# Kernel optimization log

Measured on AMD Instinct MI355X. Metric: run time of the kernel, lower is better.

## Reference

```python
import jax, jax.numpy as jnp
import numpy as np

N = 100000   # nodes
E = 1600000  # edges (avg degree 16)
F = 128      # in_feats == h_feats
G = 64       # graphs in batch
EPS = 1e-5   # GraphNorm eps


def setup_inputs() -> dict:
    key = jax.random.key(0)
    ks = jax.random.split(key, 9)
    inputs = jax.random.normal(ks[0], (N, F), dtype=jnp.float32)
    edge_index = jax.random.randint(ks[1], (2, E), 0, N, dtype=jnp.int32)
    batch = jnp.sort(jax.random.randint(ks[2], (N,), 0, G, dtype=jnp.int32))
    edge_weight = jax.random.uniform(ks[3], (E,), dtype=jnp.float32)
    scale = 1.0 / np.sqrt(F)
    W = jax.random.normal(ks[4], (F, F), dtype=jnp.float32) * scale
    b = jax.random.normal(ks[5], (F,), dtype=jnp.float32) * scale
    gn_weight = jnp.ones((F,), dtype=jnp.float32)
    gn_bias = jnp.zeros((F,), dtype=jnp.float32)
    gn_mean_scale = jnp.ones((F,), dtype=jnp.float32)
    return {"inputs": inputs, "edge_index": edge_index, "batch": batch,
            "edge_weight": edge_weight, "W": W, "b": b,
            "gn_weight": gn_weight, "gn_bias": gn_bias,
            "gn_mean_scale": gn_mean_scale}


def _gcn_block(inputs, edge_index, batch, edge_weight, W, b,
               gn_weight, gn_bias, gn_mean_scale):
    # --- GCNConv (PyG defaults: add self-loops, symmetric norm) ---
    src, dst = edge_index[0], edge_index[1]
    loop = jnp.arange(N, dtype=src.dtype)
    src_f = jnp.concatenate([src, loop])
    dst_f = jnp.concatenate([dst, loop])
    ew_f = jnp.concatenate([edge_weight, jnp.ones((N,), edge_weight.dtype)])
    deg = jax.ops.segment_sum(ew_f, dst_f, num_segments=N)
    dis = jnp.where(deg > 0, jax.lax.rsqrt(jnp.maximum(deg, 1e-30)), 0.0)
    norm = dis[src_f] * ew_f * dis[dst_f]                    # [E+N]
    xw = inputs @ W                                          # [N, F]
    msgs = norm[:, None] * xw[src_f]                         # [E+N, F]
    h = jax.ops.segment_sum(msgs, dst_f, num_segments=N) + b # [N, F]

    # --- GraphNorm (per-graph mean/std with learnable mean_scale) ---
    cnt = jnp.maximum(jax.ops.segment_sum(jnp.ones((N,), h.dtype), batch,
                                          num_segments=G), 1.0)  # [G]
    mean = jax.ops.segment_sum(h, batch, num_segments=G) / cnt[:, None]
    out = h - mean[batch] * gn_mean_scale
    var = jax.ops.segment_sum(out * out, batch, num_segments=G) / cnt[:, None]
    std = jnp.sqrt(var + EPS)
    h = gn_weight * out / std[batch] + gn_bias

    # --- ReLU, then global max pool over each graph ---
    h_emb = jax.nn.relu(h)
    flat = jax.ops.segment_max(h_emb, batch, num_segments=G)  # [G, F]
    return h_emb, flat


def reference(inputs, edge_index, batch, edge_weight, W, b,
              gn_weight, gn_bias, gn_mean_scale):
    h_emb, flat = _gcn_block(inputs, edge_index, batch, edge_weight, W, b,
                             gn_weight, gn_bias, gn_mean_scale)
    return (h_emb, flat, edge_index, edge_weight, batch)
```

## Files before the change

kernel.cpp:

```cpp
#include <hip/hip_runtime.h>

#define NN 100000
#define NE 1600000
#define FF 128
#define NG 64
#define GN_EPS 1e-5f
#define SLOT 64

typedef unsigned int uint;
typedef unsigned long long ull;
typedef unsigned short ushort;
typedef __attribute__((ext_vector_type(8))) short short8;
typedef __attribute__((ext_vector_type(4))) float f32x4;

__device__ __forceinline__ float bflo(uint u) { return __uint_as_float(u << 16); }
__device__ __forceinline__ float bfhi(uint u) { return __uint_as_float(u & 0xffff0000u); }
__device__ __forceinline__ uint f2bf1(float a) {
    uint ua = __float_as_uint(a);
    return (ua + 0x7fffu + ((ua >> 16) & 1u)) >> 16;
}
__device__ __forceinline__ uint f2bf_pack(float a, float b) {
    return f2bf1(a) | (f2bf1(b) << 16);
}

__global__ void k_init(ull* pk, float* sum1, float* sum2, int* flat_i) {
    int i = blockIdx.x * blockDim.x + threadIdx.x;
    if (i < NN) pk[i] = 0ULL;
    if (i < NG * FF) { sum1[i] = 0.f; sum2[i] = 0.f; flat_i[i] = 0; }
}

__global__ void k_deg(const int* __restrict__ ei, const float* __restrict__ ew,
                      ull* __restrict__ pk, uint* __restrict__ eslot) {
    int e = blockIdx.x * blockDim.x + threadIdx.x;
    if (e < NE) {
        int s = ei[e];
        int d = ei[NE + e];
        float w = ew[e];
        ull fx = (ull)(w * 4294967296.0f);
        ull old = atomicAdd(&pk[d], (1ULL << 48) | fx);
        int r = (int)(old >> 48);
        uint entry = ((uint)s << 15) | (uint)__float2int_rn(w * 32767.0f);
        if (r < SLOT)
            __builtin_nontemporal_store(entry, &eslot[(size_t)d * SLOT + r]);
    }
}

__global__ void k_dis(const ull* __restrict__ pk, float* __restrict__ dis,
                      int* __restrict__ indeg, const int* __restrict__ batch,
                      int* __restrict__ gstart) {
    int i = blockIdx.x * blockDim.x + threadIdx.x;
    if (i >= NN) return;
    ull p = pk[i];
    float deg = 1.0f + (float)((double)(p & 0xFFFFFFFFFFFFULL) * (1.0 / 4294967296.0));
    dis[i] = rsqrtf(deg);
    int c = (int)(p >> 48);
    indeg[i] = c < SLOT ? c : SLOT;
    int b = batch[i];
    int prev = (i == 0) ? -1 : batch[i - 1];
    for (int g = prev + 1; g <= b; g++) gstart[g] = i;
    if (i == NN - 1) { for (int g = b + 1; g <= NG; g++) gstart[g] = NN; }
}

__global__ void k_wcvt(const float* __restrict__ W, uint4* __restrict__ wb) {
    int t = blockIdx.x * blockDim.x + threadIdx.x;
    if (t >= 2048) return;
    int tile = t >> 6, l = t & 63;
    int nt = tile >> 2, kt = tile & 3;
    int j = nt * 16 + (l & 15);
    int kb = kt * 32 + (l >> 4) * 8;
    uint u[4];
    #pragma unroll
    for (int p = 0; p < 4; p++) {
        float e0 = W[(size_t)(kb + 2 * p + 0) * FF + j];
        float e1 = W[(size_t)(kb + 2 * p + 1) * FF + j];
        u[p] = f2bf_pack(e0, e1);
    }
    wb[t] = make_uint4(u[0], u[1], u[2], u[3]);
}

__global__ __launch_bounds__(256) void k_gemm(const float* __restrict__ A,
                                              const uint4* __restrict__ wb,
                                              const float* __restrict__ dis,
                                              uint* __restrict__ xwh) {
    __shared__ uint4 wlds[2048];
    int t = threadIdx.x;
    for (int i = t; i < 2048; i += 256) wlds[i] = wb[i];
    __syncthreads();

    int wave = t >> 6, lane = t & 63;
    int kg = lane >> 4;
    int row = blockIdx.x * 64 + wave * 16 + (lane & 15);
    int rowc = row < NN ? row : NN - 1;

    const float4* A4 = (const float4*)A;
    short8 afrag[4];
    #pragma unroll
    for (int kt = 0; kt < 4; kt++) {
        float4 pq0 = A4[(size_t)rowc * 32 + kt * 8 + kg * 2 + 0];
        float4 pq1 = A4[(size_t)rowc * 32 + kt * 8 + kg * 2 + 1];
        uint u0 = f2bf_pack(pq0.x, pq0.y);
        uint u1 = f2bf_pack(pq0.z, pq0.w);
        uint u2 = f2bf_pack(pq1.x, pq1.y);
        uint u3 = f2bf_pack(pq1.z, pq1.w);
        short8 f;
        f[0] = (short)(u0 & 0xffff); f[1] = (short)(u0 >> 16);
        f[2] = (short)(u1 & 0xffff); f[3] = (short)(u1 >> 16);
        f[4] = (short)(u2 & 0xffff); f[5] = (short)(u2 >> 16);
        f[6] = (short)(u3 & 0xffff); f[7] = (short)(u3 >> 16);
        afrag[kt] = f;
    }

    f32x4 acc[8];
    #pragma unroll
    for (int nt = 0; nt < 8; nt++) acc[nt] = (f32x4){0.f, 0.f, 0.f, 0.f};

    #pragma unroll
    for (int nt = 0; nt < 8; nt++) {
        #pragma unroll
        for (int kt = 0; kt < 4; kt++) {
            short8 bfrag = *(const short8*)&wlds[(nt * 4 + kt) * 64 + lane];
            acc[nt] = __builtin_amdgcn_mfma_f32_16x16x32_bf16(afrag[kt], bfrag, acc[nt], 0, 0, 0);
        }
    }

    float dv[4];
    #pragma unroll
    for (int r = 0; r < 4; r++) {
        int rout = blockIdx.x * 64 + wave * 16 + kg * 4 + r;
        dv[r] = (rout < NN) ? dis[rout] : 0.f;
    }
    ushort* xs = (ushort*)xwh;
    int col0 = lane & 15;
    #pragma unroll
    for (int nt = 0; nt < 8; nt++) {
        #pragma unroll
        for (int r = 0; r < 4; r++) {
            int rout = blockIdx.x * 64 + wave * 16 + kg * 4 + r;
            if (rout < NN)
                xs[(size_t)rout * FF + nt * 16 + col0] = (ushort)f2bf1(acc[nt][r] * dv[r]);
        }
    }
}

__global__ __launch_bounds__(256) void k_agg(const int* __restrict__ indeg,
                                             const uint* __restrict__ eslot,
                                             const uint* __restrict__ xwh,
                                             const float* __restrict__ dis,
                                             const float* __restrict__ bias,
                                             uint* __restrict__ h32) {
    int wid = (blockIdx.x * blockDim.x + threadIdx.x) >> 6;
    int lane = threadIdx.x & 63;
    if (wid >= NN) return;
    int cnt = indeg[wid];
    float dd = dis[wid];
    uint us = xwh[(size_t)wid * 64 + lane];
    float px = bflo(us), py = bfhi(us);
    const uint* base = eslot + (size_t)wid * SLOT;
    const float qs = 1.0f / 32767.0f;
    int i = 0;
    for (; i + 3 < cnt; i += 4) {
        uint4 pp = *(const uint4*)&base[i];
        uint u0 = xwh[(size_t)(pp.x >> 15) * 64 + lane];
        uint u1 = xwh[(size_t)(pp.y >> 15) * 64 + lane];
        uint u2 = xwh[(size_t)(pp.z >> 15) * 64 + lane];
        uint u3 = xwh[(size_t)(pp.w >> 15) * 64 + lane];
        float w0 = (float)(pp.x & 0x7fff) * qs;
        float w1 = (float)(pp.y & 0x7fff) * qs;
        float w2 = (float)(pp.z & 0x7fff) * qs;
        float w3 = (float)(pp.w & 0x7fff) * qs;
        px += w0 * bflo(u0); py += w0 * bfhi(u0);
        px += w1 * bflo(u1); py += w1 * bfhi(u1);
        px += w2 * bflo(u2); py += w2 * bfhi(u2);
        px += w3 * bflo(u3); py += w3 * bfhi(u3);
    }
    for (; i < cnt; i++) {
        uint p0 = base[i];
        uint u0 = xwh[(size_t)(p0 >> 15) * 64 + lane];
        float w0 = (float)(p0 & 0x7fff) * qs;
        px += w0 * bflo(u0); py += w0 * bfhi(u0);
    }
    float2 bb = ((const float2*)bias)[lane];
    h32[(size_t)wid * 64 + lane] = f2bf_pack(bb.x + dd * px, bb.y + dd * py);
}

__global__ __launch_bounds__(256) void k_gsums(const uint* __restrict__ h32,
                                               const int* __restrict__ gstart,
                                               float* __restrict__ sum1,
                                               float* __restrict__ sum2) {
    __shared__ float s1a[256], s1b[256], s2a[256], s2b[256];
    int g = blockIdx.x >> 3;
    int s = blockIdx.x & 7;
    int t = threadIdx.x;
    int f2 = t & 63;
    int half = t >> 6;
    int a = gstart[g], b = gstart[g + 1];
    float x0 = 0.f, x1 = 0.f, y0 = 0.f, y1 = 0.f;
    for (int n = a + s * 4 + half; n < b; n += 32) {
        uint u = h32[(size_t)n * 64 + f2];
        float v0 = bflo(u), v1 = bfhi(u);
        x0 += v0; x1 += v1; y0 += v0 * v0; y1 += v1 * v1;
    }
    s1a[t] = x0; s1b[t] = x1; s2a[t] = y0; s2b[t] = y1;
    __syncthreads();
    if (half == 0) {
        for (int j = 1; j < 4; j++) {
            x0 += s1a[t + j * 64]; x1 += s1b[t + j * 64];
            y0 += s2a[t + j * 64]; y1 += s2b[t + j * 64];
        }
        atomicAdd(&sum1[g * FF + f2 * 2 + 0], x0);
        atomicAdd(&sum1[g * FF + f2 * 2 + 1], x1);
        atomicAdd(&sum2[g * FF + f2 * 2 + 0], y0);
        atomicAdd(&sum2[g * FF + f2 * 2 + 1], y1);
    }
}

__global__ void k_gstats(const float* sum1, const float* sum2, const int* gstart,
                         const float* ms, float* cfac, float* istd) {
    int i = blockIdx.x * blockDim.x + threadIdx.x;
    if (i >= NG * FF) return;
    int g = i >> 7, f = i & 127;
    float cnt = (float)max(gstart[g + 1] - gstart[g], 1);
    float mean = sum1[i] / cnt;
    float c = mean * ms[f];
    float var = sum2[i] / cnt - 2.f * c * mean + c * c;
    var = fmaxf(var, 0.f);
    cfac[i] = c;
    istd[i] = rsqrtf(var + GN_EPS);
}

__global__ __launch_bounds__(256) void k_final(const uint* __restrict__ h32,
                                               const int* __restrict__ batch,
                                               const float* __restrict__ cfac,
                                               const float* __restrict__ istd,
                                               const float* __restrict__ gw,
                                               const float* __restrict__ gb,
                                               float* __restrict__ out,
                                               int* __restrict__ flat_i) {
    __shared__ float sm[8][FF];
    __shared__ int gg[8];
    int t = threadIdx.x;
    int n0 = blockIdx.x * 8;
    int rq = t >> 5;
    int q = t & 31;
    int n = n0 + rq;
    if (t < 8) gg[t] = batch[n0 + t];
    int g = batch[n];
    int fq = q * 4;
    uint2 hu = *(const uint2*)&h32[(size_t)n * 64 + q * 2];
    float4 h4 = { bflo(hu.x), bfhi(hu.x), bflo(hu.y), bfhi(hu.y) };
    float4 c4 = *(const float4*)&cfac[g * FF + fq];
    float4 s4 = *(const float4*)&istd[g * FF + fq];
    float4 w4 = *(const float4*)&gw[fq];
    float4 b4 = *(const float4*)&gb[fq];
    float4 y;
    y.x = fmaxf(w4.x * (h4.x - c4.x) * s4.x + b4.x, 0.f);
    y.y = fmaxf(w4.y * (h4.y - c4.y) * s4.y + b4.y, 0.f);
    y.z = fmaxf(w4.z * (h4.z - c4.z) * s4.z + b4.z, 0.f);
    y.w = fmaxf(w4.w * (h4.w - c4.w) * s4.w + b4.w, 0.f);
    *(float4*)&out[(size_t)n * FF + fq] = y;
    *(float4*)&sm[rq][fq] = y;
    __syncthreads();
    if (t < FF) {
        int f = t;
        int gprev = gg[0];
        float m = 0.f;
        for (int r = 0; r < 8; r++) {
            int gr = gg[r];
            if (gr != gprev) {
                atomicMax(&flat_i[gprev * FF + f], __float_as_int(m));
                m = 0.f; gprev = gr;
            }
            m = fmaxf(m, sm[r][f]);
        }
        atomicMax(&flat_i[gprev * FF + f], __float_as_int(m));
    }
}

__global__ void k_copy(const int4* __restrict__ ei4, const float4* __restrict__ ew4,
                       const int4* __restrict__ b4, float* __restrict__ out_tail) {
    int i = blockIdx.x * blockDim.x + threadIdx.x;
    if (i < 2 * NE / 4) {
        int4 v = ei4[i];
        float4 o = { (float)v.x, (float)v.y, (float)v.z, (float)v.w };
        *(float4*)&out_tail[(size_t)i * 4] = o;
    } else if (i < 2 * NE / 4 + NE / 4) {
        int j = i - 2 * NE / 4;
        *(float4*)&out_tail[2 * NE + (size_t)j * 4] = ew4[j];
    } else if (i < 2 * NE / 4 + NE / 4 + NN / 4) {
        int j = i - (2 * NE / 4 + NE / 4);
        int4 v = b4[j];
        float4 o = { (float)v.x, (float)v.y, (float)v.z, (float)v.w };
        *(float4*)&out_tail[3 * NE + (size_t)j * 4] = o;
    }
}

extern "C" void kernel_launch(void* const* d_in, const int* in_sizes, int n_in,
                              void* d_out, int out_size, void* d_ws, size_t ws_size,
                              hipStream_t stream) {
    const float* inputs = (const float*)d_in[0];
    const int*   ei     = (const int*)d_in[1];
    const int*   batch  = (const int*)d_in[2];
    const float* ew     = (const float*)d_in[3];
    const float* W      = (const float*)d_in[4];
    const float* bias   = (const float*)d_in[5];
    const float* gnw    = (const float*)d_in[6];
    const float* gnb    = (const float*)d_in[7];
    const float* ms     = (const float*)d_in[8];
    float* out = (float*)d_out;

    char* p = (char*)d_ws;
    uint* xwh    = (uint*)p;  p += (size_t)NN * 64 * 4;
    uint* h32    = (uint*)p;  p += (size_t)NN * 64 * 4;
    uint* eslot  = (uint*)p;  p += (size_t)NN * SLOT * 4;
    ull* pk      = (ull*)p;   p += (size_t)NN * 8;
    float* dis   = (float*)p; p += (size_t)NN * 4;
    float* sum1  = (float*)p; p += (size_t)NG * FF * 4;
    float* sum2  = (float*)p; p += (size_t)NG * FF * 4;
    float* cfac  = (float*)p; p += (size_t)NG * FF * 4;
    float* istd  = (float*)p; p += (size_t)NG * FF * 4;
    int* indeg   = (int*)p;   p += (size_t)NN * 4;
    int* gstart  = (int*)p;   p += (size_t)(NG + 1) * 4;
    uint4* wb    = (uint4*)p; p += 2048 * 16;

    const int TB = 256;
    int nblkN  = (NN + TB - 1) / TB;
    int nblkE  = (NE + TB - 1) / TB;

    float* out_hemb = out;
    float* out_flat = out + (size_t)NN * FF;
    float* out_tail = out_flat + (size_t)NG * FF;
    int*   flat_i   = (int*)out_flat;

    k_init<<<nblkN, TB, 0, stream>>>(pk, sum1, sum2, flat_i);
    k_deg<<<nblkE, TB, 0, stream>>>(ei, ew, pk, eslot);
    k_dis<<<nblkN, TB, 0, stream>>>(pk, dis, indeg, batch, gstart);
    k_wcvt<<<8, 256, 0, stream>>>(W, wb);
    k_gemm<<<(NN + 63) / 64, 256, 0, stream>>>(inputs, wb, dis, xwh);
    k_agg<<<NN / 4, 256, 0, stream>>>(indeg, eslot, xwh, dis, bias, h32);
    k_gsums<<<NG * 8, 256, 0, stream>>>(h32, gstart, sum1, sum2);
    k_gstats<<<(NG * FF + TB - 1) / TB, TB, 0, stream>>>(sum1, sum2, gstart, ms, cfac, istd);
    k_final<<<NN / 8, 256, 0, stream>>>(h32, batch, cfac, istd, gnw, gnb, out_hemb, flat_i);
    k_copy<<<(2 * NE / 4 + NE / 4 + NN / 4 + TB - 1) / TB, TB, 0, stream>>>(
        (const int4*)ei, (const float4*)ew, (const int4*)batch, out_tail);
}
```

Baseline: 391.7 us.

## Replace global atomics with partial buffers and 32-bit degree counters

Degree accumulation now uses a 32-bit counter atomic, and the degree is recomputed from the quantized weights stored in the edge slots instead of a packed 64-bit fixed-point atomic. Per-graph sums are written to per-block partial buffers and reduced in the stats kernel, replacing float atomics. The fused max-pool in the final kernel is split into a separate two-stage reduction that rereads the output embedding. This removes atomics but adds two launches, a full extra read of the 51MB output, and slightly different degree precision, since the quantized weights drop edges beyond SLOT.

```diff
diff --git a/kernel.cpp b/kernel.cpp
--- a/kernel.cpp
+++ b/kernel.cpp
@@ -23,38 +23,38 @@
     return f2bf1(a) | (f2bf1(b) << 16);
 }
 
-__global__ void k_init(ull* pk, float* sum1, float* sum2, int* flat_i) {
-    int i = blockIdx.x * blockDim.x + threadIdx.x;
-    if (i < NN) pk[i] = 0ULL;
-    if (i < NG * FF) { sum1[i] = 0.f; sum2[i] = 0.f; flat_i[i] = 0; }
+__global__ void k_init(uint* cnt) {
+    int i = blockIdx.x * blockDim.x + threadIdx.x;
+    if (i < NN) cnt[i] = 0u;
 }
 
 __global__ void k_deg(const int* __restrict__ ei, const float* __restrict__ ew,
-                      ull* __restrict__ pk, uint* __restrict__ eslot) {
+                      uint* __restrict__ cnt, uint* __restrict__ eslot) {
     int e = blockIdx.x * blockDim.x + threadIdx.x;
     if (e < NE) {
         int s = ei[e];
         int d = ei[NE + e];
         float w = ew[e];
-        ull fx = (ull)(w * 4294967296.0f);
-        ull old = atomicAdd(&pk[d], (1ULL << 48) | fx);
-        int r = (int)(old >> 48);
+        uint r = atomicAdd(&cnt[d], 1u);
         uint entry = ((uint)s << 15) | (uint)__float2int_rn(w * 32767.0f);
         if (r < SLOT)
             __builtin_nontemporal_store(entry, &eslot[(size_t)d * SLOT + r]);
     }
 }
 
-__global__ void k_dis(const ull* __restrict__ pk, float* __restrict__ dis,
-                      int* __restrict__ indeg, const int* __restrict__ batch,
-                      int* __restrict__ gstart) {
+__global__ void k_dis(const uint* __restrict__ cnt, const uint* __restrict__ eslot,
+                      float* __restrict__ dis, int* __restrict__ indeg,
+                      const int* __restrict__ batch, int* __restrict__ gstart) {
     int i = blockIdx.x * blockDim.x + threadIdx.x;
     if (i >= NN) return;
-    ull p = pk[i];
-    float deg = 1.0f + (float)((double)(p & 0xFFFFFFFFFFFFULL) * (1.0 / 4294967296.0));
-    dis[i] = rsqrtf(deg);
-    int c = (int)(p >> 48);
-    indeg[i] = c < SLOT ? c : SLOT;
+    uint c0 = cnt[i];
+    int c = c0 < SLOT ? (int)c0 : SLOT;
+    indeg[i] = c;
+    const uint* base = eslot + (size_t)i * SLOT;
+    float s = 0.f;
+    const float qs = 1.0f / 32767.0f;
+    for (int j = 0; j < c; j++) s += (float)(base[j] & 0x7fff);
+    dis[i] = rsqrtf(1.0f + s * qs);
     int b = batch[i];
     int prev = (i == 0) ? -1 : batch[i - 1];
     for (int g = prev + 1; g <= b; g++) gstart[g] = i;
@@ -185,8 +185,8 @@
 
 __global__ __launch_bounds__(256) void k_gsums(const uint* __restrict__ h32,
                                                const int* __restrict__ gstart,
-                                               float* __restrict__ sum1,
-                                               float* __restrict__ sum2) {
+                                               float* __restrict__ psum1,
+                                               float* __restrict__ psum2) {
     __shared__ float s1a[256], s1b[256], s2a[256], s2b[256];
     int g = blockIdx.x >> 3;
     int s = blockIdx.x & 7;
@@ -207,22 +207,28 @@
             x0 += s1a[t + j * 64]; x1 += s1b[t + j * 64];
             y0 += s2a[t + j * 64]; y1 += s2b[t + j * 64];
         }
-        atomicAdd(&sum1[g * FF + f2 * 2 + 0], x0);
-        atomicAdd(&sum1[g * FF + f2 * 2 + 1], x1);
-        atomicAdd(&sum2[g * FF + f2 * 2 + 0], y0);
-        atomicAdd(&sum2[g * FF + f2 * 2 + 1], y1);
-    }
-}
-
-__global__ void k_gstats(const float* sum1, const float* sum2, const int* gstart,
-                         const float* ms, float* cfac, float* istd) {
+        int bse = blockIdx.x * FF + f2 * 2;
+        psum1[bse + 0] = x0; psum1[bse + 1] = x1;
+        psum2[bse + 0] = y0; psum2[bse + 1] = y1;
+    }
+}
+
+__global__ void k_gstats(const float* __restrict__ psum1, const float* __restrict__ psum2,
+                         const int* gstart, const float* ms,
+                         float* cfac, float* istd) {
     int i = blockIdx.x * blockDim.x + threadIdx.x;
     if (i >= NG * FF) return;
     int g = i >> 7, f = i & 127;
-    float cnt = (float)max(gstart[g + 1] - gstart[g], 1);
-    float mean = sum1[i] / cnt;
+    float s1 = 0.f, s2 = 0.f;
+    #pragma unroll
+    for (int s = 0; s < 8; s++) {
+        s1 += psum1[(g * 8 + s) * FF + f];
+        s2 += psum2[(g * 8 + s) * FF + f];
+    }
+    float cntf = (float)max(gstart[g + 1] - gstart[g], 1);
+    float mean = s1 / cntf;
     float c = mean * ms[f];
-    float var = sum2[i] / cnt - 2.f * c * mean + c * c;
+    float var = s2 / cntf - 2.f * c * mean + c * c;
     var = fmaxf(var, 0.f);
     cfac[i] = c;
     istd[i] = rsqrtf(var + GN_EPS);
@@ -234,18 +240,13 @@
                                                const float* __restrict__ istd,
                                                const float* __restrict__ gw,
                                                const float* __restrict__ gb,
-                                               float* __restrict__ out,
-                                               int* __restrict__ flat_i) {
-    __shared__ float sm[8][FF];
-    __shared__ int gg[8];
-    int t = threadIdx.x;
-    int n0 = blockIdx.x * 8;
-    int rq = t >> 5;
-    int q = t & 31;
-    int n = n0 + rq;
-    if (t < 8) gg[t] = batch[n0 + t];
+                                               float* __restrict__ out) {
+    int i = blockIdx.x * blockDim.x + threadIdx.x;
+    if (i >= NN * 32) return;
+    int n = i >> 5;
+    int q = i & 31;
+    int fq = q * 4;
     int g = batch[n];
-    int fq = q * 4;
     uint2 hu = *(const uint2*)&h32[(size_t)n * 64 + q * 2];
     float4 h4 = { bflo(hu.x), bfhi(hu.x), bflo(hu.y), bfhi(hu.y) };
     float4 c4 = *(const float4*)&cfac[g * FF + fq];
@@ -258,22 +259,35 @@
     y.z = fmaxf(w4.z * (h4.z - c4.z) * s4.z + b4.z, 0.f);
     y.w = fmaxf(w4.w * (h4.w - c4.w) * s4.w + b4.w, 0.f);
     *(float4*)&out[(size_t)n * FF + fq] = y;
-    *(float4*)&sm[rq][fq] = y;
+}
+
+__global__ __launch_bounds__(256) void k_gmax(const float* __restrict__ hemb,
+                                              const int* __restrict__ gstart,
+                                              float* __restrict__ pmax) {
+    __shared__ float sm[256];
+    int g = blockIdx.x >> 3;
+    int s = blockIdx.x & 7;
+    int t = threadIdx.x;
+    int f = t & 127, rr = t >> 7;
+    int a = gstart[g], b = gstart[g + 1];
+    float m = 0.f;
+    for (int n = a + s * 2 + rr; n < b; n += 16)
+        m = fmaxf(m, hemb[(size_t)n * FF + f]);
+    sm[t] = m;
     __syncthreads();
-    if (t < FF) {
-        int f = t;
-        int gprev = gg[0];
-        float m = 0.f;
-        for (int r = 0; r < 8; r++) {
-            int gr = gg[r];
-            if (gr != gprev) {
-                atomicMax(&flat_i[gprev * FF + f], __float_as_int(m));
-                m = 0.f; gprev = gr;
-            }
-            m = fmaxf(m, sm[r][f]);
-        }
-        atomicMax(&flat_i[gprev * FF + f], __float_as_int(m));
-    }
+    if (rr == 0)
+        pmax[blockIdx.x * FF + f] = fmaxf(sm[t], sm[t + 128]);
+}
+
+__global__ void k_gmax2(const float* __restrict__ pmax, float* __restrict__ flat) {
+    int i = blockIdx.x * blockDim.x + threadIdx.x;
+    if (i >= NG * FF) return;
+    int g = i >> 7, f = i & 127;
+    float m = 0.f;
+    #pragma unroll
+    for (int s = 0; s < 8; s++)
+        m = fmaxf(m, pmax[(g * 8 + s) * FF + f]);
+    flat[i] = m;
 }
 
 __global__ void k_copy(const int4* __restrict__ ei4, const float4* __restrict__ ew4,
@@ -312,10 +326,11 @@
     uint* xwh    = (uint*)p;  p += (size_t)NN * 64 * 4;
     uint* h32    = (uint*)p;  p += (size_t)NN * 64 * 4;
     uint* eslot  = (uint*)p;  p += (size_t)NN * SLOT * 4;
-    ull* pk      = (ull*)p;   p += (size_t)NN * 8;
+    uint* cnt    = (uint*)p;  p += (size_t)NN * 4;
     float* dis   = (float*)p; p += (size_t)NN * 4;
-    float* sum1  = (float*)p; p += (size_t)NG * FF * 4;
-    float* sum2  = (float*)p; p += (size_t)NG * FF * 4;
+    float* psum1 = (float*)p; p += (size_t)NG * 8 * FF * 4;
+    float* psum2 = (float*)p; p += (size_t)NG * 8 * FF * 4;
+    float* pmax  = (float*)p; p += (size_t)NG * 8 * FF * 4;
     float* cfac  = (float*)p; p += (size_t)NG * FF * 4;
     float* istd  = (float*)p; p += (size_t)NG * FF * 4;
     int* indeg   = (int*)p;   p += (size_t)NN * 4;
@@ -329,17 +344,18 @@
     float* out_hemb = out;
     float* out_flat = out + (size_t)NN * FF;
     float* out_tail = out_flat + (size_t)NG * FF;
-    int*   flat_i   = (int*)out_flat;
-
-    k_init<<<nblkN, TB, 0, stream>>>(pk, sum1, sum2, flat_i);
-    k_deg<<<nblkE, TB, 0, stream>>>(ei, ew, pk, eslot);
-    k_dis<<<nblkN, TB, 0, stream>>>(pk, dis, indeg, batch, gstart);
+
+    k_init<<<nblkN, TB, 0, stream>>>(cnt);
+    k_deg<<<nblkE, TB, 0, stream>>>(ei, ew, cnt, eslot);
+    k_dis<<<nblkN, TB, 0, stream>>>(cnt, eslot, dis, indeg, batch, gstart);
     k_wcvt<<<8, 256, 0, stream>>>(W, wb);
     k_gemm<<<(NN + 63) / 64, 256, 0, stream>>>(inputs, wb, dis, xwh);
     k_agg<<<NN / 4, 256, 0, stream>>>(indeg, eslot, xwh, dis, bias, h32);
-    k_gsums<<<NG * 8, 256, 0, stream>>>(h32, gstart, sum1, sum2);
-    k_gstats<<<(NG * FF + TB - 1) / TB, TB, 0, stream>>>(sum1, sum2, gstart, ms, cfac, istd);
-    k_final<<<NN / 8, 256, 0, stream>>>(h32, batch, cfac, istd, gnw, gnb, out_hemb, flat_i);
+    k_gsums<<<NG * 8, 256, 0, stream>>>(h32, gstart, psum1, psum2);
+    k_gstats<<<(NG * FF + TB - 1) / TB, TB, 0, stream>>>(psum1, psum2, gstart, ms, cfac, istd);
+    k_final<<<(NN * 32 + TB - 1) / TB, TB, 0, stream>>>(h32, batch, cfac, istd, gnw, gnb, out_hemb);
+    k_gmax<<<NG * 8, 256, 0, stream>>>(out_hemb, gstart, pmax);
+    k_gmax2<<<(NG * FF + TB - 1) / TB, TB, 0, stream>>>(pmax, out_flat);
     k_copy<<<(2 * NE / 4 + NE / 4 + NN / 4 + TB - 1) / TB, TB, 0, stream>>>(
         (const int4*)ei, (const float4*)ew, (const int4*)batch, out_tail);
 }
```

Measured after the change: 407.2 us. 4.0% more time.

## Replace global per-node atomics with two-pass bucketed edge partition for CSR build

Applied to the files above, without the earlier changes.

Builds the padded per-destination edge lists in two passes. First, edges are binned by destination block of 128 nodes into a staging buffer using LDS histograms and one global atomic per bucket per block. Then each bucket is scattered locally with LDS atomics. Degree is now recomputed from the quantized slot weights instead of 64-bit fixed-point atomics, and the W conversion is folded into k_dis. GraphNorm sums are written as partials instead of float atomics, which makes them deterministic. The costs are an extra pass over the staging buffer, which aliases h32, and a degree that is wrong if a bucket overflows CAP or a node has more than 64 in-edges.

```diff
diff --git a/kernel.cpp b/kernel.cpp
--- a/kernel.cpp
+++ b/kernel.cpp
@@ -6,9 +6,11 @@
 #define NG 64
 #define GN_EPS 1e-5f
 #define SLOT 64
+#define NB 782
+#define CAP 2560
+#define PBLK 256
 
 typedef unsigned int uint;
-typedef unsigned long long ull;
 typedef unsigned short ushort;
 typedef __attribute__((ext_vector_type(8))) short short8;
 typedef __attribute__((ext_vector_type(4))) float f32x4;
@@ -23,59 +25,95 @@
     return f2bf1(a) | (f2bf1(b) << 16);
 }
 
-__global__ void k_init(ull* pk, float* sum1, float* sum2, int* flat_i) {
-    int i = blockIdx.x * blockDim.x + threadIdx.x;
-    if (i < NN) pk[i] = 0ULL;
-    if (i < NG * FF) { sum1[i] = 0.f; sum2[i] = 0.f; flat_i[i] = 0; }
-}
-
-__global__ void k_deg(const int* __restrict__ ei, const float* __restrict__ ew,
-                      ull* __restrict__ pk, uint* __restrict__ eslot) {
-    int e = blockIdx.x * blockDim.x + threadIdx.x;
-    if (e < NE) {
+__global__ __launch_bounds__(256) void k_part(const int* __restrict__ ei,
+                                              const float* __restrict__ ew,
+                                              uint* __restrict__ gfill,
+                                              uint2* __restrict__ ebuf) {
+    __shared__ uint hist[1024], base[1024];
+    int tid = threadIdx.x;
+    int e0 = blockIdx.x * (NE / PBLK);
+    int e1 = e0 + (NE / PBLK);
+    for (int c = tid; c < 1024; c += 256) hist[c] = 0;
+    __syncthreads();
+    for (int e = e0 + tid; e < e1; e += 256) {
+        int d = ei[NE + e];
+        atomicAdd(&hist[d >> 7], 1u);
+    }
+    __syncthreads();
+    for (int c = tid; c < 1024; c += 256) {
+        uint h = hist[c];
+        base[c] = (c < NB && h) ? atomicAdd(&gfill[c * 16], h) : 0u;
+        hist[c] = 0;
+    }
+    __syncthreads();
+    for (int e = e0 + tid; e < e1; e += 256) {
         int s = ei[e];
         int d = ei[NE + e];
         float w = ew[e];
-        ull fx = (ull)(w * 4294967296.0f);
-        ull old = atomicAdd(&pk[d], (1ULL << 48) | fx);
-        int r = (int)(old >> 48);
-        uint entry = ((uint)s << 15) | (uint)__float2int_rn(w * 32767.0f);
+        int b = d >> 7;
+        uint r = atomicAdd(&hist[b], 1u);
+        uint pos = base[b] + r;
+        if (pos < CAP)
+            ebuf[(size_t)b * CAP + pos] =
+                make_uint2((uint)s | ((uint)(d & 127) << 17), __float_as_uint(w));
+    }
+}
+
+__global__ __launch_bounds__(256) void k_build(const uint* __restrict__ gfill,
+                                               const uint2* __restrict__ ebuf,
+                                               uint* __restrict__ eslot,
+                                               uint* __restrict__ cnt) {
+    __shared__ uint lcnt[128];
+    int b = blockIdx.x;
+    int tid = threadIdx.x;
+    if (tid < 128) lcnt[tid] = 0;
+    __syncthreads();
+    uint m = gfill[b * 16]; if (m > CAP) m = CAP;
+    int n0 = b << 7;
+    for (uint i = tid; i < m; i += 256) {
+        uint2 en = ebuf[(size_t)b * CAP + i];
+        uint src = en.x & 0x1FFFFu;
+        uint dlo = (en.x >> 17) & 127u;
+        float w = __uint_as_float(en.y);
+        uint r = atomicAdd(&lcnt[dlo], 1u);
         if (r < SLOT)
-            __builtin_nontemporal_store(entry, &eslot[(size_t)d * SLOT + r]);
-    }
-}
-
-__global__ void k_dis(const ull* __restrict__ pk, float* __restrict__ dis,
-                      int* __restrict__ indeg, const int* __restrict__ batch,
-                      int* __restrict__ gstart) {
+            eslot[(size_t)(n0 + dlo) * SLOT + r] =
+                (src << 15) | (uint)__float2int_rn(w * 32767.0f);
+    }
+    __syncthreads();
+    if (tid < 128 && n0 + tid < NN) cnt[n0 + tid] = lcnt[tid];
+}
+
+__global__ void k_dis(const uint* __restrict__ cnt, const uint* __restrict__ eslot,
+                      float* __restrict__ dis, const int* __restrict__ batch,
+                      int* __restrict__ gstart, const float* __restrict__ W,
+                      uint4* __restrict__ wb) {
     int i = blockIdx.x * blockDim.x + threadIdx.x;
+    if (i < 2048) {
+        int tile = i >> 6, l = i & 63;
+        int nt = tile >> 2, kt = tile & 3;
+        int j = nt * 16 + (l & 15);
+        int kb = kt * 32 + (l >> 4) * 8;
+        uint u[4];
+        #pragma unroll
+        for (int p = 0; p < 4; p++) {
+            float e0 = W[(size_t)(kb + 2 * p + 0) * FF + j];
+            float e1 = W[(size_t)(kb + 2 * p + 1) * FF + j];
+            u[p] = f2bf_pack(e0, e1);
+        }
+        wb[i] = make_uint4(u[0], u[1], u[2], u[3]);
+    }
     if (i >= NN) return;
-    ull p = pk[i];
-    float deg = 1.0f + (float)((double)(p & 0xFFFFFFFFFFFFULL) * (1.0 / 4294967296.0));
-    dis[i] = rsqrtf(deg);
-    int c = (int)(p >> 48);
-    indeg[i] = c < SLOT ? c : SLOT;
+    uint c0 = cnt[i];
+    int c = c0 < SLOT ? (int)c0 : SLOT;
+    const uint* base = eslot + (size_t)i * SLOT;
+    float s = 0.f;
+    for (int j = 0; j < c; j++) s += (float)(base[j] & 0x7fff);
+    dis[i] = rsqrtf(1.0f + s * (1.0f / 32767.0f));
     int b = batch[i];
     int prev = (i == 0) ? -1 : batch[i - 1];
     for (int g = prev + 1; g <= b; g++) gstart[g] = i;
     if (i == NN - 1) { for (int g = b + 1; g <= NG; g++) gstart[g] = NN; }
-}
-
-__global__ void k_wcvt(const float* __restrict__ W, uint4* __restrict__ wb) {
-    int t = blockIdx.x * blockDim.x + threadIdx.x;
-    if (t >= 2048) return;
-    int tile = t >> 6, l = t & 63;
-    int nt = tile >> 2, kt = tile & 3;
-    int j = nt * 16 + (l & 15);
-    int kb = kt * 32 + (l >> 4) * 8;
-    uint u[4];
-    #pragma unroll
-    for (int p = 0; p < 4; p++) {
-        float e0 = W[(size_t)(kb + 2 * p + 0) * FF + j];
-        float e1 = W[(size_t)(kb + 2 * p + 1) * FF + j];
-        u[p] = f2bf_pack(e0, e1);
-    }
-    wb[t] = make_uint4(u[0], u[1], u[2], u[3]);
 }
 
 __global__ __launch_bounds__(256) void k_gemm(const float* __restrict__ A,
@@ -142,7 +180,7 @@
     }
 }
 
-__global__ __launch_bounds__(256) void k_agg(const int* __restrict__ indeg,
+__global__ __launch_bounds__(256) void k_agg(const uint* __restrict__ cnt,
                                              const uint* __restrict__ eslot,
                                              const uint* __restrict__ xwh,
                                              const float* __restrict__ dis,
@@ -151,14 +189,15 @@
     int wid = (blockIdx.x * blockDim.x + threadIdx.x) >> 6;
     int lane = threadIdx.x & 63;
     if (wid >= NN) return;
-    int cnt = indeg[wid];
+    uint c0 = cnt[wid];
+    int c = c0 < SLOT ? (int)c0 : SLOT;
     float dd = dis[wid];
     uint us = xwh[(size_t)wid * 64 + lane];
     float px = bflo(us), py = bfhi(us);
     const uint* base = eslot + (size_t)wid * SLOT;
     const float qs = 1.0f / 32767.0f;
     int i = 0;
-    for (; i + 3 < cnt; i += 4) {
+    for (; i + 3 < c; i += 4) {
         uint4 pp = *(const uint4*)&base[i];
         uint u0 = xwh[(size_t)(pp.x >> 15) * 64 + lane];
         uint u1 = xwh[(size_t)(pp.y >> 15) * 64 + lane];
@@ -173,7 +212,7 @@
         px += w2 * bflo(u2); py += w2 * bfhi(u2);
         px += w3 * bflo(u3); py += w3 * bfhi(u3);
     }
-    for (; i < cnt; i++) {
+    for (; i < c; i++) {
         uint p0 = base[i];
         uint u0 = xwh[(size_t)(p0 >> 15) * 64 + lane];
         float w0 = (float)(p0 & 0x7fff) * qs;
@@ -185,8 +224,8 @@
 
 __global__ __launch_bounds__(256) void k_gsums(const uint* __restrict__ h32,
                                                const int* __restrict__ gstart,
-                                               float* __restrict__ sum1,
-                                               float* __restrict__ sum2) {
+                                               float* __restrict__ psum1,
+                                               float* __restrict__ psum2) {
     __shared__ float s1a[256], s1b[256], s2a[256], s2b[256];
     int g = blockIdx.x >> 3;
     int s = blockIdx.x & 7;
@@ -207,22 +246,28 @@
             x0 += s1a[t + j * 64]; x1 += s1b[t + j * 64];
             y0 += s2a[t + j * 64]; y1 += s2b[t + j * 64];
         }
-        atomicAdd(&sum1[g * FF + f2 * 2 + 0], x0);
-        atomicAdd(&sum1[g * FF + f2 * 2 + 1], x1);
-        atomicAdd(&sum2[g * FF + f2 * 2 + 0], y0);
-        atomicAdd(&sum2[g * FF + f2 * 2 + 1], y1);
-    }
-}
-
-__global__ void k_gstats(const float* sum1, const float* sum2, const int* gstart,
-                         const float* ms, float* cfac, float* istd) {
+        int bse = blockIdx.x * FF + f2 * 2;
+        psum1[bse + 0] = x0; psum1[bse + 1] = x1;
+        psum2[bse + 0] = y0; psum2[bse + 1] = y1;
+    }
+}
+
+__global__ void k_gstats(const float* __restrict__ psum1, const float* __restrict__ psum2,
+                         const int* gstart, const float* ms,
+                         float* cfac, float* istd) {
     int i = blockIdx.x * blockDim.x + threadIdx.x;
     if (i >= NG * FF) return;
     int g = i >> 7, f = i & 127;
-    float cnt = (float)max(gstart[g + 1] - gstart[g], 1);
-    float mean = sum1[i] / cnt;
+    float s1 = 0.f, s2 = 0.f;
+    #pragma unroll
+    for (int s = 0; s < 8; s++) {
+        s1 += psum1[(g * 8 + s) * FF + f];
+        s2 += psum2[(g * 8 + s) * FF + f];
+    }
+    float cntf = (float)max(gstart[g + 1] - gstart[g], 1);
+    float mean = s1 / cntf;
     float c = mean * ms[f];
-    float var = sum2[i] / cnt - 2.f * c * mean + c * c;
+    float var = s2 / cntf - 2.f * c * mean + c * c;
     var = fmaxf(var, 0.f);
     cfac[i] = c;
     istd[i] = rsqrtf(var + GN_EPS);
@@ -310,35 +355,36 @@
 
     char* p = (char*)d_ws;
     uint* xwh    = (uint*)p;  p += (size_t)NN * 64 * 4;
-    uint* h32    = (uint*)p;  p += (size_t)NN * 64 * 4;
+    uint* h32    = (uint*)p;
+    uint2* ebuf  = (uint2*)p; p += (size_t)NN * 64 * 4;
     uint* eslot  = (uint*)p;  p += (size_t)NN * SLOT * 4;
-    ull* pk      = (ull*)p;   p += (size_t)NN * 8;
+    uint* gfill  = (uint*)p;  p += (size_t)1024 * 16 * 4;
+    uint* cnt    = (uint*)p;  p += (size_t)NN * 4;
     float* dis   = (float*)p; p += (size_t)NN * 4;
-    float* sum1  = (float*)p; p += (size_t)NG * FF * 4;
-    float* sum2  = (float*)p; p += (size_t)NG * FF * 4;
+    float* psum1 = (float*)p; p += (size_t)NG * 8 * FF * 4;
+    float* psum2 = (float*)p; p += (size_t)NG * 8 * FF * 4;
     float* cfac  = (float*)p; p += (size_t)NG * FF * 4;
     float* istd  = (float*)p; p += (size_t)NG * FF * 4;
-    int* indeg   = (int*)p;   p += (size_t)NN * 4;
     int* gstart  = (int*)p;   p += (size_t)(NG + 1) * 4;
     uint4* wb    = (uint4*)p; p += 2048 * 16;
 
     const int TB = 256;
-    int nblkN  = (NN + TB - 1) / TB;
-    int nblkE  = (NE + TB - 1) / TB;
+    int nblkN = (NN + TB - 1) / TB;
 
     float* out_hemb = out;
     float* out_flat = out + (size_t)NN * FF;
     float* out_tail = out_flat + (size_t)NG * FF;
     int*   flat_i   = (int*)out_flat;
 
-    k_init<<<nblkN, TB, 0, stream>>>(pk, sum1, sum2, flat_i);
-    k_deg<<<nblkE, TB, 0, stream>>>(ei, ew, pk, eslot);
-    k_dis<<<nblkN, TB, 0, stream>>>(pk, dis, indeg, batch, gstart);
-    k_wcvt<<<8, 256, 0, stream>>>(W, wb);
+    hipMemsetAsync(gfill, 0, 1024 * 16 * 4, stream);
+    hipMemsetAsync(flat_i, 0, NG * FF * 4, stream);
+    k_part<<<PBLK, 256, 0, stream>>>(ei, ew, gfill, ebuf);
+    k_build<<<NB, 256, 0, stream>>>(gfill, ebuf, eslot, cnt);
+    k_dis<<<nblkN, TB, 0, stream>>>(cnt, eslot, dis, batch, gstart, W, wb);
     k_gemm<<<(NN + 63) / 64, 256, 0, stream>>>(inputs, wb, dis, xwh);
-    k_agg<<<NN / 4, 256, 0, stream>>>(indeg, eslot, xwh, dis, bias, h32);
-    k_gsums<<<NG * 8, 256, 0, stream>>>(h32, gstart, sum1, sum2);
-    k_gstats<<<(NG * FF + TB - 1) / TB, TB, 0, stream>>>(sum1, sum2, gstart, ms, cfac, istd);
+    k_agg<<<NN / 4, 256, 0, stream>>>(cnt, eslot, xwh, dis, bias, h32);
+    k_gsums<<<NG * 8, 256, 0, stream>>>(h32, gstart, psum1, psum2);
+    k_gstats<<<(NG * FF + TB - 1) / TB, TB, 0, stream>>>(psum1, psum2, gstart, ms, cfac, istd);
     k_final<<<NN / 8, 256, 0, stream>>>(h32, batch, cfac, istd, gnw, gnb, out_hemb, flat_i);
     k_copy<<<(2 * NE / 4 + NE / 4 + NN / 4 + TB - 1) / TB, TB, 0, stream>>>(
         (const int4*)ei, (const float4*)ew, (const int4*)batch, out_tail);
```

Measured after the change: 333.9 us. -14.8%, faster.
